# Kernel tuning notes

Hardware: AMD Instinct MI355X
Metric: run time of the kernel (lower is better)

The kernel has to match this reference:

```python
import jax, jax.numpy as jnp
import numpy as np

D_MODEL = 1024
N_HEAD = 16
ATT_DIM = D_MODEL // N_HEAD  # 64
B, S = 8, 2048


def setup_inputs() -> dict:
    key = jax.random.key(0)
    kq, kk, kv, kwq, kwk, kwv = jax.random.split(key, 6)
    # xavier_uniform bound for Linear(hidden_dim -> att_dim)
    bound = float(np.sqrt(6.0 / (D_MODEL + ATT_DIM)))
    return {
        "q": jax.random.normal(kq, (B, S, D_MODEL), dtype=jnp.float32),
        "k": jax.random.normal(kk, (B, S, D_MODEL), dtype=jnp.float32),
        "v": jax.random.normal(kv, (B, S, D_MODEL), dtype=jnp.float32),
        "Wq": jax.random.uniform(kwq, (ATT_DIM, D_MODEL), jnp.float32, -bound, bound),
        "Wk": jax.random.uniform(kwk, (ATT_DIM, D_MODEL), jnp.float32, -bound, bound),
        "Wv": jax.random.uniform(kwv, (ATT_DIM, D_MODEL), jnp.float32, -bound, bound),
    }


def reference(q, k, v, Wq, Wk, Wv):
    # Linear projections (no bias): [B,S,d_model] @ [d_model,att_dim]
    qp = jnp.einsum('bsd,ed->bse', q, Wq)
    kp = jnp.einsum('bsd,ed->bse', k, Wk)
    vp = jnp.einsum('bsd,ed->bse', v, Wv)
    # Scores: note original divides by att_dim (not sqrt)
    scores = jnp.einsum('bqe,bke->bqk', qp, kp) / ATT_DIM
    probs = jax.nn.softmax(scores, axis=-1)  # [B,S,S]
    att = jnp.einsum('bqk,bke->bqe', probs, vp)  # [B,S,att_dim]
    # dropout is identity in eval mode
    return (att, probs)
```

## Files before the change

### kernel.cpp

```cpp
#include <hip/hip_runtime.h>
#include <hip/hip_bf16.h>

#define D_MODEL 1024
#define ATT_DIM 64
#define BATCH 8
#define SEQ 2048
#define MROWS (BATCH * SEQ)

typedef short bf16x8 __attribute__((ext_vector_type(8)));
typedef float f32x4 __attribute__((ext_vector_type(4)));

#define MFMA16(a, b, c) __builtin_amdgcn_mfma_f32_16x16x32_bf16((a), (b), (c), 0, 0, 0)

__device__ inline short f2bf(float f) {
    union { __hip_bfloat16 h; short s; } u;
    u.h = __float2bfloat16(f);
    return u.s;
}

__device__ __forceinline__ unsigned cvtpk(float lo, float hi) {
    unsigned r;
    asm("v_cvt_pk_bf16_f32 %0, %1, %2" : "=v"(r) : "v"(lo), "v"(hi));
    return r;
}

__device__ __forceinline__ void gload_lds16(const void* g, void* l) {
    __builtin_amdgcn_global_load_lds(
        (const __attribute__((address_space(1))) void*)g,
        (__attribute__((address_space(3))) void*)l, 16, 0, 0);
}

__global__ __launch_bounds__(256) void wcvt_kernel(
    const float* __restrict__ Wq, const float* __restrict__ Wk,
    const float* __restrict__ Wv, short* __restrict__ Wbf)
{
    const int idx = blockIdx.x * 256 + threadIdx.x;
    const int per = ATT_DIM * D_MODEL;
    const int base = idx * 8;
    const int mi = base / per;
    const int off = base - mi * per;
    const float* src = (mi == 0) ? Wq : (mi == 1 ? Wk : Wv);
    const float sc = (mi == 0) ? (1.0f / 64.0f) : 1.0f;
    const float4 a = *reinterpret_cast<const float4*>(src + off);
    const float4 b = *reinterpret_cast<const float4*>(src + off + 4);
    bf16x8 r;
    r[0] = f2bf(a.x * sc); r[1] = f2bf(a.y * sc);
    r[2] = f2bf(a.z * sc); r[3] = f2bf(a.w * sc);
    r[4] = f2bf(b.x * sc); r[5] = f2bf(b.y * sc);
    r[6] = f2bf(b.z * sc); r[7] = f2bf(b.w * sc);
    *reinterpret_cast<bf16x8*>(Wbf + base) = r;
}

__global__ __launch_bounds__(256) void proj_mfma_kernel(
    const float* __restrict__ q, const float* __restrict__ k,
    const float* __restrict__ v, const short* __restrict__ Wbf,
    short* __restrict__ qp, short* __restrict__ kp, short* __restrict__ vpT)
{
    const int mat = blockIdx.y;
    const float* x = (mat == 0) ? q : (mat == 1 ? k : v);
    const short* W = Wbf + mat * ATT_DIM * D_MODEL;

    __shared__ float As[2][4096];

    const int tid = threadIdx.x;
    const int w = tid >> 6;
    const int l = tid & 63;
    const int lr = l & 15;
    const int g = l >> 4;

    const int m0 = blockIdx.x * 64;
    const int row = w * 16 + lr;
    const int xr = (row & 7) << 4;

    f32x4 acc[4] = {};

    #define STAGE(c, buf)                                                      \
        {                                                                      \
            const int kt_ = (c) * 64;                                          \
            _Pragma("unroll")                                                  \
            for (int j = 0; j < 4; ++j) {                                      \
                const int rs = (w * 4 + j) * 4 + g;                            \
                const int scb = (lr * 16) ^ ((rs & 7) << 4);                   \
                gload_lds16(x + (long)(m0 + rs) * D_MODEL + kt_ + (scb >> 2),  \
                            &As[buf][(w * 4 + j) * 256]);                      \
            }                                                                  \
        }

    STAGE(0, 0);
    __syncthreads();

    for (int c = 0; c < 16; ++c) {
        const int buf = c & 1;
        if (c < 15) STAGE(c + 1, buf ^ 1);

        const int kt = c * 64;
        const char* Ab = (const char*)&As[buf][0] + row * 256;
        #pragma unroll
        for (int ks = 0; ks < 2; ++ks) {
            const int b0 = ks * 128 + g * 32;
            const float4 a0 = *reinterpret_cast<const float4*>(Ab + (b0 ^ xr));
            const float4 a1 = *reinterpret_cast<const float4*>(Ab + ((b0 + 16) ^ xr));
            bf16x8 af;
            af[0] = f2bf(a0.x); af[1] = f2bf(a0.y); af[2] = f2bf(a0.z); af[3] = f2bf(a0.w);
            af[4] = f2bf(a1.x); af[5] = f2bf(a1.y); af[6] = f2bf(a1.z); af[7] = f2bf(a1.w);
            #pragma unroll
            for (int ef = 0; ef < 4; ++ef) {
                const bf16x8 wf = *reinterpret_cast<const bf16x8*>(
                    W + (ef * 16 + lr) * D_MODEL + kt + ks * 32 + g * 8);
                acc[ef] = MFMA16(af, wf, acc[ef]);
            }
        }
        __syncthreads();
    }
    #undef STAGE

    if (mat < 2) {
        short* out = (mat == 0) ? qp : kp;
        #pragma unroll
        for (int ef = 0; ef < 4; ++ef)
            #pragma unroll
            for (int j = 0; j < 4; ++j)
                out[(long)(m0 + w * 16 + g * 4 + j) * ATT_DIM + ef * 16 + lr] =
                    f2bf(acc[ef][j]);
    } else {
        const int b = m0 / SEQ;
        const int s0 = (m0 - b * SEQ) + w * 16;
        #pragma unroll
        for (int ef = 0; ef < 4; ++ef)
            #pragma unroll
            for (int j = 0; j < 4; ++j)
                vpT[((long)b * ATT_DIM + ef * 16 + lr) * SEQ + s0 + g * 4 + j] =
                    f2bf(acc[ef][j]);
    }
}

union AttnSmem {
    float panel[8][16][128];
    float o[8][64][17];
};

__global__ __launch_bounds__(512, 4) void attn_kernel(
    const short* __restrict__ qp, const short* __restrict__ kp,
    const short* __restrict__ vpT, float* __restrict__ probs,
    float* __restrict__ att)
{
    __shared__ __align__(16) AttnSmem u;
    __shared__ float stats_l[8][16];

    const int tid = threadIdx.x;
    const int w = tid >> 6;
    const int l = tid & 63;
    const int lr = l & 15;
    const int g = l >> 4;

    const int b = blockIdx.y;
    const int q0 = blockIdx.x * 16;

    const short* qpb = qp + ((long)b * SEQ + q0) * ATT_DIM;
    const short* kpb = kp + (long)b * SEQ * ATT_DIM;
    const short* vTb = vpT + (long)b * ATT_DIM * SEQ;

    const bf16x8 qa0 = *reinterpret_cast<const bf16x8*>(qpb + lr * ATT_DIM + g * 8);
    const bf16x8 qa1 = *reinterpret_cast<const bf16x8*>(qpb + lr * ATT_DIM + 32 + g * 8);

    const int kbeg = w * 256;

    f32x4 s[8][2];
    #pragma unroll
    for (int ch = 0; ch < 8; ++ch) {
        const short* kb = kpb + (long)(kbeg + ch * 32) * ATT_DIM;
        const bf16x8 kb00 = *reinterpret_cast<const bf16x8*>(kb + lr * ATT_DIM + g * 8);
        const bf16x8 kb01 = *reinterpret_cast<const bf16x8*>(kb + lr * ATT_DIM + 32 + g * 8);
        const bf16x8 kb10 = *reinterpret_cast<const bf16x8*>(kb + (16 + lr) * ATT_DIM + g * 8);
        const bf16x8 kb11 = *reinterpret_cast<const bf16x8*>(kb + (16 + lr) * ATT_DIM + 32 + g * 8);
        f32x4 t0 = {}; t0 = MFMA16(kb00, qa0, t0); t0 = MFMA16(kb01, qa1, t0);
        f32x4 t1 = {}; t1 = MFMA16(kb10, qa0, t1); t1 = MFMA16(kb11, qa1, t1);
        s[ch][0] = t0; s[ch][1] = t1;
    }

    float lw = 0.f;
    #pragma unroll
    for (int ch = 0; ch < 8; ++ch)
        #pragma unroll
        for (int h = 0; h < 2; ++h)
            #pragma unroll
            for (int j = 0; j < 4; ++j) {
                const float e = __expf(s[ch][h][j]);
                s[ch][h][j] = e;
                lw += e;
            }
    lw += __shfl_xor(lw, 16);
    lw += __shfl_xor(lw, 32);

    if (l < 16) stats_l[w][l] = lw;
    __syncthreads();

    float tot = 0.f;
    #pragma unroll
    for (int ww = 0; ww < 8; ++ww) tot += stats_l[ww][lr];
    const float inv = 1.0f / tot;
    #pragma unroll
    for (int ch = 0; ch < 8; ++ch)
        #pragma unroll
        for (int h = 0; h < 2; ++h)
            s[ch][h] *= inv;

    f32x4 accO[4] = {};
    const bool hi2 = (g & 2) != 0;
    const bool swp = ((g ^ (g >> 1)) & 1) != 0;
    const bool odd = (g & 1) != 0;

    #pragma unroll
    for (int ch = 0; ch < 8; ++ch) {
        const int k0 = kbeg + ch * 32;

        {
            const int c0 = (ch & 3) * 32 + g * 4;
            char* base = (char*)&u.panel[w][0][0] + lr * 512;
            *reinterpret_cast<f32x4*>(base + ((c0 * 4) ^ ((lr & 7) << 4))) = s[ch][0];
            *reinterpret_cast<f32x4*>(base + (((c0 + 16) * 4) ^ ((lr & 7) << 4))) = s[ch][1];
        }

        const unsigned xy0 = cvtpk(s[ch][0][0], s[ch][0][1]);
        const unsigned xy1 = cvtpk(s[ch][0][2], s[ch][0][3]);
        const unsigned zw0 = cvtpk(s[ch][1][0], s[ch][1][1]);
        const unsigned zw1 = cvtpk(s[ch][1][2], s[ch][1][3]);

        const unsigned s1a = hi2 ? xy0 : zw0;
        const unsigned s1b = hi2 ? xy1 : zw1;
        const unsigned r1a = __shfl_xor(s1a, 32);
        const unsigned r1b = __shfl_xor(s1b, 32);
        const unsigned p1a = hi2 ? zw0 : xy0;
        const unsigned p1b = hi2 ? zw1 : xy1;
        const unsigned s2a = swp ? p1a : r1a;
        const unsigned s2b = swp ? p1b : r1b;
        const unsigned r2a = __shfl_xor(s2a, 16);
        const unsigned r2b = __shfl_xor(s2b, 16);
        const unsigned ka = swp ? r1a : p1a;
        const unsigned kb_ = swp ? r1b : p1b;
        const unsigned d0 = odd ? r2a : ka;
        const unsigned d1 = odd ? r2b : kb_;
        const unsigned d2 = odd ? ka : r2a;
        const unsigned d3 = odd ? kb_ : r2b;
        union { uint4 u4; bf16x8 v; } pbu;
        pbu.u4 = make_uint4(d0, d1, d2, d3);
        const bf16x8 pb = pbu.v;

        #pragma unroll
        for (int ef = 0; ef < 4; ++ef) {
            const bf16x8 va = *reinterpret_cast<const bf16x8*>(
                vTb + (long)(ef * 16 + lr) * SEQ + k0 + g * 8);
            accO[ef] = MFMA16(va, pb, accO[ef]);
        }

        if ((ch & 3) == 3) {
            const int half = ch >> 2;
            #pragma unroll
            for (int j = 0; j < 8; ++j) {
                const int r = j * 2 + (l >> 5);
                const int cb = ((l & 31) * 16) ^ ((r & 7) << 4);
                const f32x4 val = *reinterpret_cast<const f32x4*>(
                    (const char*)&u.panel[w][0][0] + r * 512 + cb);
                *reinterpret_cast<f32x4*>(
                    probs + ((long)b * SEQ + q0 + r) * SEQ + kbeg + half * 128 +
                    (l & 31) * 4) = val;
            }
        }
    }

    __syncthreads();
    #pragma unroll
    for (int ef = 0; ef < 4; ++ef)
        #pragma unroll
        for (int j = 0; j < 4; ++j)
            u.o[w][ef * 16 + g * 4 + j][lr] = accO[ef][j];
    __syncthreads();

    {
        const int qr = tid >> 5;
        const int e0 = (tid & 31) * 2;
        float o0 = 0.f, o1 = 0.f;
        #pragma unroll
        for (int ww = 0; ww < 8; ++ww) {
            o0 += u.o[ww][e0][qr];
            o1 += u.o[ww][e0 + 1][qr];
        }
        float2 o = make_float2(o0, o1);
        *reinterpret_cast<float2*>(att + ((long)b * SEQ + q0 + qr) * ATT_DIM + e0) = o;
    }
}

extern "C" void kernel_launch(void* const* d_in, const int* in_sizes, int n_in,
                              void* d_out, int out_size, void* d_ws, size_t ws_size,
                              hipStream_t stream)
{
    const float* q  = (const float*)d_in[0];
    const float* k  = (const float*)d_in[1];
    const float* v  = (const float*)d_in[2];
    const float* Wq = (const float*)d_in[3];
    const float* Wk = (const float*)d_in[4];
    const float* Wv = (const float*)d_in[5];

    float* att   = (float*)d_out;
    float* probs = att + (size_t)BATCH * SEQ * ATT_DIM;

    short* qp  = (short*)d_ws;
    short* kp  = qp + (size_t)MROWS * ATT_DIM;
    short* vpT = kp + (size_t)MROWS * ATT_DIM;
    short* Wbf = vpT + (size_t)MROWS * ATT_DIM;

    wcvt_kernel<<<dim3(96), 256, 0, stream>>>(Wq, Wk, Wv, Wbf);

    proj_mfma_kernel<<<dim3(MROWS / 64, 3), 256, 0, stream>>>(
        q, k, v, Wbf, qp, kp, vpT);

    attn_kernel<<<dim3(SEQ / 16, BATCH), 512, 0, stream>>>(
        qp, kp, vpT, probs, att);
}
```

Measured before the change: 144.9 us.

## Split projection GEMM over K across waves with partial-sum merge kernel

The projection kernel now gives each of its four waves a quarter of the reduction dimension for a 16-row tile. Inputs are read straight from global memory into registers, with no LDS staging. Each wave writes fp32 partial sums to a workspace, and a new merge kernel adds the four partials, converts to bf16, and transposes V through LDS. This is meant to raise parallelism and drop LDS pipelining and sync overhead, at the cost of extra partial-sum traffic (12 fp32 copies of the projections) and an added kernel launch.

```diff
diff --git a/kernel.cpp b/kernel.cpp
--- a/kernel.cpp
+++ b/kernel.cpp
@@ -22,12 +22,6 @@
     unsigned r;
     asm("v_cvt_pk_bf16_f32 %0, %1, %2" : "=v"(r) : "v"(lo), "v"(hi));
     return r;
-}
-
-__device__ __forceinline__ void gload_lds16(const void* g, void* l) {
-    __builtin_amdgcn_global_load_lds(
-        (const __attribute__((address_space(1))) void*)g,
-        (__attribute__((address_space(3))) void*)l, 16, 0, 0);
 }
 
 __global__ __launch_bounds__(256) void wcvt_kernel(
@@ -51,16 +45,14 @@
     *reinterpret_cast<bf16x8*>(Wbf + base) = r;
 }
 
-__global__ __launch_bounds__(256) void proj_mfma_kernel(
+__global__ __launch_bounds__(256, 8) void proj_part_kernel(
     const float* __restrict__ q, const float* __restrict__ k,
     const float* __restrict__ v, const short* __restrict__ Wbf,
-    short* __restrict__ qp, short* __restrict__ kp, short* __restrict__ vpT)
+    float* __restrict__ part)
 {
     const int mat = blockIdx.y;
     const float* x = (mat == 0) ? q : (mat == 1 ? k : v);
     const short* W = Wbf + mat * ATT_DIM * D_MODEL;
-
-    __shared__ float As[2][4096];
 
     const int tid = threadIdx.x;
     const int w = tid >> 6;
@@ -68,69 +60,80 @@
     const int lr = l & 15;
     const int g = l >> 4;
 
+    const int m0 = blockIdx.x * 16;
+    const int kq = w * 256;
+
+    const float* xrow = x + (long)(m0 + lr) * D_MODEL + kq + g * 8;
+    const short* wb0 = W + (0 * 16 + lr) * D_MODEL + kq + g * 8;
+    const short* wb1 = W + (1 * 16 + lr) * D_MODEL + kq + g * 8;
+    const short* wb2 = W + (2 * 16 + lr) * D_MODEL + kq + g * 8;
+    const short* wb3 = W + (3 * 16 + lr) * D_MODEL + kq + g * 8;
+
+    f32x4 acc[4] = {};
+
+    #pragma unroll
+    for (int c = 0; c < 8; ++c) {
+        const float4 a0 = *reinterpret_cast<const float4*>(xrow + c * 32);
+        const float4 a1 = *reinterpret_cast<const float4*>(xrow + c * 32 + 4);
+        union { uint4 u4; bf16x8 v8; } afu;
+        afu.u4.x = cvtpk(a0.x, a0.y);
+        afu.u4.y = cvtpk(a0.z, a0.w);
+        afu.u4.z = cvtpk(a1.x, a1.y);
+        afu.u4.w = cvtpk(a1.z, a1.w);
+        const bf16x8 af = afu.v8;
+        acc[0] = MFMA16(af, *reinterpret_cast<const bf16x8*>(wb0 + c * 32), acc[0]);
+        acc[1] = MFMA16(af, *reinterpret_cast<const bf16x8*>(wb1 + c * 32), acc[1]);
+        acc[2] = MFMA16(af, *reinterpret_cast<const bf16x8*>(wb2 + c * 32), acc[2]);
+        acc[3] = MFMA16(af, *reinterpret_cast<const bf16x8*>(wb3 + c * 32), acc[3]);
+    }
+
+    float* pout = part + ((long)(mat * 4 + w) * MROWS) * ATT_DIM;
+    #pragma unroll
+    for (int ef = 0; ef < 4; ++ef)
+        #pragma unroll
+        for (int j = 0; j < 4; ++j)
+            pout[(long)(m0 + g * 4 + j) * ATT_DIM + ef * 16 + lr] = acc[ef][j];
+}
+
+__global__ __launch_bounds__(256) void proj_merge_kernel(
+    const float* __restrict__ part,
+    short* __restrict__ qp, short* __restrict__ kp, short* __restrict__ vpT)
+{
+    __shared__ float vt[64][65];
+
+    const int mat = blockIdx.y;
     const int m0 = blockIdx.x * 64;
-    const int row = w * 16 + lr;
-    const int xr = (row & 7) << 4;
-
-    f32x4 acc[4] = {};
-
-    #define STAGE(c, buf)                                                      \
-        {                                                                      \
-            const int kt_ = (c) * 64;                                          \
-            _Pragma("unroll")                                                  \
-            for (int j = 0; j < 4; ++j) {                                      \
-                const int rs = (w * 4 + j) * 4 + g;                            \
-                const int scb = (lr * 16) ^ ((rs & 7) << 4);                   \
-                gload_lds16(x + (long)(m0 + rs) * D_MODEL + kt_ + (scb >> 2),  \
-                            &As[buf][(w * 4 + j) * 256]);                      \
-            }                                                                  \
-        }
-
-    STAGE(0, 0);
-    __syncthreads();
-
-    for (int c = 0; c < 16; ++c) {
-        const int buf = c & 1;
-        if (c < 15) STAGE(c + 1, buf ^ 1);
-
-        const int kt = c * 64;
-        const char* Ab = (const char*)&As[buf][0] + row * 256;
-        #pragma unroll
-        for (int ks = 0; ks < 2; ++ks) {
-            const int b0 = ks * 128 + g * 32;
-            const float4 a0 = *reinterpret_cast<const float4*>(Ab + (b0 ^ xr));
-            const float4 a1 = *reinterpret_cast<const float4*>(Ab + ((b0 + 16) ^ xr));
-            bf16x8 af;
-            af[0] = f2bf(a0.x); af[1] = f2bf(a0.y); af[2] = f2bf(a0.z); af[3] = f2bf(a0.w);
-            af[4] = f2bf(a1.x); af[5] = f2bf(a1.y); af[6] = f2bf(a1.z); af[7] = f2bf(a1.w);
-            #pragma unroll
-            for (int ef = 0; ef < 4; ++ef) {
-                const bf16x8 wf = *reinterpret_cast<const bf16x8*>(
-                    W + (ef * 16 + lr) * D_MODEL + kt + ks * 32 + g * 8);
-                acc[ef] = MFMA16(af, wf, acc[ef]);
-            }
-        }
-        __syncthreads();
-    }
-    #undef STAGE
+    const int tid = threadIdx.x;
+
+    const float* p0 = part + ((long)(mat * 4 + 0) * MROWS + m0) * ATT_DIM;
+    const float* p1 = part + ((long)(mat * 4 + 1) * MROWS + m0) * ATT_DIM;
+    const float* p2 = part + ((long)(mat * 4 + 2) * MROWS + m0) * ATT_DIM;
+    const float* p3 = part + ((long)(mat * 4 + 3) * MROWS + m0) * ATT_DIM;
 
     if (mat < 2) {
         short* out = (mat == 0) ? qp : kp;
         #pragma unroll
-        for (int ef = 0; ef < 4; ++ef)
-            #pragma unroll
-            for (int j = 0; j < 4; ++j)
-                out[(long)(m0 + w * 16 + g * 4 + j) * ATT_DIM + ef * 16 + lr] =
-                    f2bf(acc[ef][j]);
+        for (int i = 0; i < 16; ++i) {
+            const int idx = i * 256 + tid;
+            const float s = p0[idx] + p1[idx] + p2[idx] + p3[idx];
+            out[(long)m0 * ATT_DIM + idx] = f2bf(s);
+        }
     } else {
+        #pragma unroll
+        for (int i = 0; i < 16; ++i) {
+            const int idx = i * 256 + tid;
+            const int row = idx >> 6, e = idx & 63;
+            vt[e][row] = p0[idx] + p1[idx] + p2[idx] + p3[idx];
+        }
+        __syncthreads();
         const int b = m0 / SEQ;
-        const int s0 = (m0 - b * SEQ) + w * 16;
-        #pragma unroll
-        for (int ef = 0; ef < 4; ++ef)
-            #pragma unroll
-            for (int j = 0; j < 4; ++j)
-                vpT[((long)b * ATT_DIM + ef * 16 + lr) * SEQ + s0 + g * 4 + j] =
-                    f2bf(acc[ef][j]);
+        const int s0 = m0 - b * SEQ;
+        #pragma unroll
+        for (int i = 0; i < 16; ++i) {
+            const int idx = i * 256 + tid;
+            const int e = idx >> 6, so = idx & 63;
+            vpT[((long)b * ATT_DIM + e) * SEQ + s0 + so] = f2bf(vt[e][so]);
+        }
     }
 }
 
@@ -308,11 +311,15 @@
     short* kp  = qp + (size_t)MROWS * ATT_DIM;
     short* vpT = kp + (size_t)MROWS * ATT_DIM;
     short* Wbf = vpT + (size_t)MROWS * ATT_DIM;
+    float* part = (float*)(Wbf + (size_t)3 * ATT_DIM * D_MODEL);
 
     wcvt_kernel<<<dim3(96), 256, 0, stream>>>(Wq, Wk, Wv, Wbf);
 
-    proj_mfma_kernel<<<dim3(MROWS / 64, 3), 256, 0, stream>>>(
-        q, k, v, Wbf, qp, kp, vpT);
+    proj_part_kernel<<<dim3(MROWS / 16, 3), 256, 0, stream>>>(
+        q, k, v, Wbf, part);
+
+    proj_merge_kernel<<<dim3(MROWS / 64, 3), 256, 0, stream>>>(
+        part, qp, kp, vpT);
 
     attn_kernel<<<dim3(SEQ / 16, BATCH), 512, 0, stream>>>(
         qp, kp, vpT, probs, att);
```

New measurement: 181.8 us. +25.5%, slower.
